# Kernel tuning notes

Hardware: AMD Instinct MI355X
Metric: run time of the kernel (lower is better)

## Reference

```python
import jax, jax.numpy as jnp
import numpy as np

WINDOW_SIZE = 11
N_CHANNELS = 3
SIGMA = 1.5
K1, K2 = 0.01, 0.03
VALUE_RANGE = 1.0


def _create_window(window_size: int, n_channels: int, sigma: float) -> np.ndarray:
    # 1D gaussian, normalized, then outer product -> 2D kernel
    coords = np.arange(window_size, dtype=np.float32) - (window_size - 1) / 2.0
    g = np.exp(-(coords ** 2) / (2.0 * sigma ** 2))
    g = g / g.sum()
    k2d = np.outer(g, g).astype(np.float32)  # (K, K), sums to 1
    # depthwise kernel, OIHW with I=1 (groups = n_channels)
    return np.broadcast_to(k2d, (n_channels, 1, window_size, window_size)).copy()


def _dwconv(x, window):
    # depthwise valid conv, NCHW / OIHW
    return jax.lax.conv_general_dilated(
        x, window, window_strides=(1, 1), padding='VALID',
        feature_group_count=window.shape[0],
        dimension_numbers=('NCHW', 'OIHW', 'NCHW'))


def setup_inputs() -> dict:
    key = jax.random.key(0)
    kx, ky = jax.random.split(key)
    N, C, H, W = 32, N_CHANNELS, 512, 512
    x = jax.random.uniform(kx, (N, C, H, W), dtype=jnp.float32)
    y = jax.random.uniform(ky, (N, C, H, W), dtype=jnp.float32)
    window = jnp.asarray(_create_window(WINDOW_SIZE, N_CHANNELS, SIGMA))
    return {"x": x, "y": y, "window": window}


def reference(x, y, window):
    c1 = (K1 * VALUE_RANGE) ** 2
    c2 = (K2 * VALUE_RANGE) ** 2

    mu_x = _dwconv(x, window)
    mu_y = _dwconv(y, window)
    mu_x_sq = mu_x ** 2
    mu_y_sq = mu_y ** 2
    mu_xy = mu_x * mu_y

    sigma_x_sq = _dwconv(x * x, window) - mu_x_sq
    sigma_y_sq = _dwconv(y * y, window) - mu_y_sq
    sigma_xy = _dwconv(x * y, window) - mu_xy

    cs = (2.0 * sigma_xy + c2) / (sigma_x_sq + sigma_y_sq + c2)
    ss = (2.0 * mu_xy + c1) / (mu_x_sq + mu_y_sq + c1) * cs

    l = ss.mean(axis=(-1, -2))  # (N, C) per-channel SSIM
    l = l.mean(axis=-1)         # (N,)  per-sample
    return l.mean()             # reduction='mean'
```

## Files before the change

kernel.cpp:

```cpp
#include <hip/hip_runtime.h>

#define KS    11
#define HH    512
#define WW    512
#define OUTD  502
#define OH    34
#define ROWS  44
#define NB    15
#define NIMG  96
#define PADW  524

__global__ __launch_bounds__(256, 2)
void ssim_main(const float* __restrict__ xg, const float* __restrict__ yg,
               const float* __restrict__ win, double* __restrict__ acc_out)
{
    __shared__ float xs[2][PADW];
    __shared__ float ys[2][PADW];
    __shared__ float wsums[4];

    const int tid  = threadIdx.x;
    const int img  = blockIdx.x % NIMG;
    const int band = blockIdx.x / NIMG;
    const int row0 = band * OH;
    const int c0   = 2 * tid;

    float g[KS];
    #pragma unroll
    for (int i = 0; i < KS; i++) {
        float s = 0.f;
        #pragma unroll
        for (int j = 0; j < KS; j++) s += win[i * KS + j];
        g[i] = s;
    }

    if (tid < (PADW - WW)) {
        xs[0][WW + tid] = 0.f; xs[1][WW + tid] = 0.f;
        ys[0][WW + tid] = 0.f; ys[1][WW + tid] = 0.f;
    }

    const float* xi = xg + (size_t)img * HH * WW;
    const float* yi = yg + (size_t)img * HH * WW;

    float acc[5][2][KS];
    #pragma unroll
    for (int q = 0; q < 5; q++)
        #pragma unroll
        for (int c = 0; c < 2; c++)
            #pragma unroll
            for (int s = 0; s < KS; s++) acc[q][c][s] = 0.f;

    float ssum = 0.f;

    const float C1 = 0.0001f;
    const float C2 = 0.0009f;

    float2 vx, vy;
    {
        int gr = row0; if (gr > HH - 1) gr = HH - 1;
        vx = *(const float2*)&xi[(size_t)gr * WW + c0];
        vy = *(const float2*)&yi[(size_t)gr * WW + c0];
        xs[0][c0] = vx.x; xs[0][c0 + 1] = vx.y;
        ys[0][c0] = vy.x; ys[0][c0 + 1] = vy.y;
        gr = row0 + 1; if (gr > HH - 1) gr = HH - 1;
        vx = *(const float2*)&xi[(size_t)gr * WW + c0];
        vy = *(const float2*)&yi[(size_t)gr * WW + c0];
    }
    __syncthreads();

    #pragma unroll 1
    for (int rb = 0; rb < ROWS / KS; rb++) {
        #pragma unroll
        for (int rr = 0; rr < KS; rr++) {
            const int r = rb * KS + rr;

            const float* xb = xs[r & 1];
            const float* yb = ys[r & 1];
            float xv[12], yv[12];
            #pragma unroll
            for (int k = 0; k < 6; k++) {
                float2 a = *(const float2*)&xb[c0 + 2 * k];
                float2 b = *(const float2*)&yb[c0 + 2 * k];
                xv[2 * k] = a.x; xv[2 * k + 1] = a.y;
                yv[2 * k] = b.x; yv[2 * k + 1] = b.y;
            }

            if (r + 1 < ROWS) {
                float* xw = xs[(r + 1) & 1];
                float* yw = ys[(r + 1) & 1];
                xw[c0] = vx.x; xw[c0 + 1] = vx.y;
                yw[c0] = vy.x; yw[c0 + 1] = vy.y;
            }
            if (r + 2 < ROWS) {
                int gr = row0 + r + 2; if (gr > HH - 1) gr = HH - 1;
                vx = *(const float2*)&xi[(size_t)gr * WW + c0];
                vy = *(const float2*)&yi[(size_t)gr * WW + c0];
            }

            float xx[12], yy[12], xy[12];
            #pragma unroll
            for (int k = 0; k < 12; k++) {
                xx[k] = xv[k] * xv[k];
                yy[k] = yv[k] * yv[k];
                xy[k] = xv[k] * yv[k];
            }

            float h[5][2];
            #pragma unroll
            for (int q = 0; q < 5; q++) { h[q][0] = 0.f; h[q][1] = 0.f; }
            #pragma unroll
            for (int j = 0; j < KS; j++) {
                const float gj = g[j];
                h[0][0] = fmaf(gj, xv[j], h[0][0]); h[0][1] = fmaf(gj, xv[j + 1], h[0][1]);
                h[1][0] = fmaf(gj, yv[j], h[1][0]); h[1][1] = fmaf(gj, yv[j + 1], h[1][1]);
                h[2][0] = fmaf(gj, xx[j], h[2][0]); h[2][1] = fmaf(gj, xx[j + 1], h[2][1]);
                h[3][0] = fmaf(gj, yy[j], h[3][0]); h[3][1] = fmaf(gj, yy[j + 1], h[3][1]);
                h[4][0] = fmaf(gj, xy[j], h[4][0]); h[4][1] = fmaf(gj, xy[j + 1], h[4][1]);
            }

            #pragma unroll
            for (int i = 0; i < KS; i++) {
                const int slot = (rr - i + KS) % KS;
                const float gi = g[i];
                #pragma unroll
                for (int q = 0; q < 5; q++) {
                    acc[q][0][slot] = fmaf(gi, h[q][0], acc[q][0][slot]);
                    acc[q][1][slot] = fmaf(gi, h[q][1], acc[q][1][slot]);
                }
            }

            const int es   = (rr + 1) % KS;
            const int jloc = r - (KS - 1);
            if (jloc >= 0 && (row0 + jloc) < OUTD) {
                #pragma unroll
                for (int c = 0; c < 2; c++) {
                    if (c0 + c < OUTD) {
                        const float mx  = acc[0][c][es], my  = acc[1][c][es];
                        const float Sxx = acc[2][c][es], Syy = acc[3][c][es], Sxy = acc[4][c][es];
                        const float mxx = mx * mx, myy = my * my, mxy = mx * my;
                        const float sxx = Sxx - mxx, syy = Syy - myy, sxy = Sxy - mxy;
                        const float num = (2.f * mxy + C1) * (2.f * sxy + C2);
                        const float den = (mxx + myy + C1) * (sxx + syy + C2);
                        float rc = __builtin_amdgcn_rcpf(den);
                        rc = rc * fmaf(-den, rc, 2.0f);
                        ssum = fmaf(num, rc, ssum);
                    }
                }
            }
            #pragma unroll
            for (int q = 0; q < 5; q++) { acc[q][0][es] = 0.f; acc[q][1][es] = 0.f; }

            __syncthreads();
        }
    }

    #pragma unroll
    for (int off = 32; off > 0; off >>= 1)
        ssum += __shfl_down(ssum, off);
    const int wave = tid >> 6;
    if ((tid & 63) == 0) wsums[wave] = ssum;
    __syncthreads();
    if (tid == 0) {
        float s = wsums[0] + wsums[1] + wsums[2] + wsums[3];
        atomicAdd(acc_out, (double)s);
    }
}

__global__ void ssim_finalize(const double* __restrict__ acc, float* __restrict__ out)
{
    out[0] = (float)(acc[0] * (1.0 / 24192384.0));
}

extern "C" void kernel_launch(void* const* d_in, const int* in_sizes, int n_in,
                              void* d_out, int out_size, void* d_ws, size_t ws_size,
                              hipStream_t stream)
{
    const float* x   = (const float*)d_in[0];
    const float* y   = (const float*)d_in[1];
    const float* win = (const float*)d_in[2];
    float* out = (float*)d_out;
    double* acc = (double*)d_ws;

    hipMemsetAsync(acc, 0, sizeof(double), stream);
    ssim_main<<<dim3(NIMG * NB), dim3(256), 0, stream>>>(x, y, win, acc);
    ssim_finalize<<<dim3(1), dim3(1), 0, stream>>>(acc, out);
}
```

Measured before the change: 278.7 us.

## Use packed float2 FMAs, one column per thread, and split images into column tiles

Each thread now handles one output column instead of two, and each image band is split into two 256-column tiles, which doubles the grid. The x and y values are interleaved into a single shared buffer of float2 pairs. The horizontal and vertical passes use packed two-wide FMAs on (x,y) pairs, which lets the compiler emit v_pk_fma_f32. Per-thread register state shrinks, so launch bounds go from 2 to 3 blocks per CU to raise occupancy. The trade-off is redundant halo loads at tile edges and fewer columns per thread to amortise the shared-memory reads.

```diff
diff --git a/kernel.cpp b/kernel.cpp
--- a/kernel.cpp
+++ b/kernel.cpp
@@ -1,4 +1,6 @@
 #include <hip/hip_runtime.h>
+
+typedef float v2f __attribute__((ext_vector_type(2)));
 
 #define KS    11
 #define HH    512
@@ -6,23 +8,26 @@
 #define OUTD  502
 #define OH    34
 #define ROWS  44
-#define NB    15
+#define NBR   15
+#define NBC   2
+#define TC    256
+#define SG    266
 #define NIMG  96
-#define PADW  524
 
-__global__ __launch_bounds__(256, 2)
+__global__ __launch_bounds__(256, 3)
 void ssim_main(const float* __restrict__ xg, const float* __restrict__ yg,
                const float* __restrict__ win, double* __restrict__ acc_out)
 {
-    __shared__ float xs[2][PADW];
-    __shared__ float ys[2][PADW];
+    __shared__ v2f buf[2][SG];
     __shared__ float wsums[4];
 
-    const int tid  = threadIdx.x;
-    const int img  = blockIdx.x % NIMG;
-    const int band = blockIdx.x / NIMG;
-    const int row0 = band * OH;
-    const int c0   = 2 * tid;
+    const int tid = threadIdx.x;
+    int bb = blockIdx.x;
+    const int img   = bb % NIMG;  bb /= NIMG;
+    const int band  = bb % NBR;   bb /= NBR;
+    const int ctile = bb;
+    const int row0  = band * OH;
+    const int cb    = ctile * TC;
 
     float g[KS];
     #pragma unroll
@@ -33,38 +38,41 @@
         g[i] = s;
     }
 
-    if (tid < (PADW - WW)) {
-        xs[0][WW + tid] = 0.f; xs[1][WW + tid] = 0.f;
-        ys[0][WW + tid] = 0.f; ys[1][WW + tid] = 0.f;
-    }
-
     const float* xi = xg + (size_t)img * HH * WW;
     const float* yi = yg + (size_t)img * HH * WW;
 
-    float acc[5][2][KS];
+    v2f   aMu[KS], aSq[KS];
+    float aXy[KS];
     #pragma unroll
-    for (int q = 0; q < 5; q++)
-        #pragma unroll
-        for (int c = 0; c < 2; c++)
-            #pragma unroll
-            for (int s = 0; s < KS; s++) acc[q][c][s] = 0.f;
+    for (int s = 0; s < KS; s++) {
+        aMu[s] = (v2f)0.f; aSq[s] = (v2f)0.f; aXy[s] = 0.f;
+    }
 
     float ssum = 0.f;
-
     const float C1 = 0.0001f;
     const float C2 = 0.0009f;
 
-    float2 vx, vy;
-    {
-        int gr = row0; if (gr > HH - 1) gr = HH - 1;
-        vx = *(const float2*)&xi[(size_t)gr * WW + c0];
-        vy = *(const float2*)&yi[(size_t)gr * WW + c0];
-        xs[0][c0] = vx.x; xs[0][c0 + 1] = vx.y;
-        ys[0][c0] = vy.x; ys[0][c0 + 1] = vy.y;
-        gr = row0 + 1; if (gr > HH - 1) gr = HH - 1;
-        vx = *(const float2*)&xi[(size_t)gr * WW + c0];
-        vy = *(const float2*)&yi[(size_t)gr * WW + c0];
-    }
+    float px0, py0, px1, py1;
+    auto load_row = [&](int r, float& x0, float& y0, float& x1, float& y1) {
+        int gr = row0 + r; if (gr > HH - 1) gr = HH - 1;
+        const size_t base = (size_t)gr * WW;
+        const int gc0 = cb + tid;
+        x0 = xi[base + gc0]; y0 = yi[base + gc0];
+        x1 = 0.f; y1 = 0.f;
+        if (tid < SG - TC) {
+            const int gc1 = cb + TC + tid;
+            if (gc1 < WW) { x1 = xi[base + gc1]; y1 = yi[base + gc1]; }
+        }
+    };
+    auto store_row = [&](int bsel, float x0, float y0, float x1, float y1) {
+        v2f v; v.x = x0; v.y = y0;
+        buf[bsel][tid] = v;
+        if (tid < SG - TC) { v2f w; w.x = x1; w.y = y1; buf[bsel][TC + tid] = w; }
+    };
+
+    load_row(0, px0, py0, px1, py1);
+    store_row(0, px0, py0, px1, py1);
+    load_row(1, px0, py0, px1, py1);
     __syncthreads();
 
     #pragma unroll 1
@@ -72,82 +80,46 @@
         #pragma unroll
         for (int rr = 0; rr < KS; rr++) {
             const int r = rb * KS + rr;
+            const v2f* bufr = buf[r & 1];
 
-            const float* xb = xs[r & 1];
-            const float* yb = ys[r & 1];
-            float xv[12], yv[12];
-            #pragma unroll
-            for (int k = 0; k < 6; k++) {
-                float2 a = *(const float2*)&xb[c0 + 2 * k];
-                float2 b = *(const float2*)&yb[c0 + 2 * k];
-                xv[2 * k] = a.x; xv[2 * k + 1] = a.y;
-                yv[2 * k] = b.x; yv[2 * k + 1] = b.y;
-            }
+            if (r + 1 < ROWS) store_row((r + 1) & 1, px0, py0, px1, py1);
+            if (r + 2 < ROWS) load_row(r + 2, px0, py0, px1, py1);
 
-            if (r + 1 < ROWS) {
-                float* xw = xs[(r + 1) & 1];
-                float* yw = ys[(r + 1) & 1];
-                xw[c0] = vx.x; xw[c0 + 1] = vx.y;
-                yw[c0] = vy.x; yw[c0 + 1] = vy.y;
-            }
-            if (r + 2 < ROWS) {
-                int gr = row0 + r + 2; if (gr > HH - 1) gr = HH - 1;
-                vx = *(const float2*)&xi[(size_t)gr * WW + c0];
-                vy = *(const float2*)&yi[(size_t)gr * WW + c0];
-            }
-
-            float xx[12], yy[12], xy[12];
-            #pragma unroll
-            for (int k = 0; k < 12; k++) {
-                xx[k] = xv[k] * xv[k];
-                yy[k] = yv[k] * yv[k];
-                xy[k] = xv[k] * yv[k];
-            }
-
-            float h[5][2];
-            #pragma unroll
-            for (int q = 0; q < 5; q++) { h[q][0] = 0.f; h[q][1] = 0.f; }
+            v2f hMu = (v2f)0.f, hSq = (v2f)0.f;
+            float hXy = 0.f;
             #pragma unroll
             for (int j = 0; j < KS; j++) {
-                const float gj = g[j];
-                h[0][0] = fmaf(gj, xv[j], h[0][0]); h[0][1] = fmaf(gj, xv[j + 1], h[0][1]);
-                h[1][0] = fmaf(gj, yv[j], h[1][0]); h[1][1] = fmaf(gj, yv[j + 1], h[1][1]);
-                h[2][0] = fmaf(gj, xx[j], h[2][0]); h[2][1] = fmaf(gj, xx[j + 1], h[2][1]);
-                h[3][0] = fmaf(gj, yy[j], h[3][0]); h[3][1] = fmaf(gj, yy[j + 1], h[3][1]);
-                h[4][0] = fmaf(gj, xy[j], h[4][0]); h[4][1] = fmaf(gj, xy[j + 1], h[4][1]);
+                const v2f v = bufr[tid + j];
+                v2f gg; gg.x = g[j]; gg.y = g[j];
+                hMu = __builtin_elementwise_fma(gg, v, hMu);
+                const v2f sq = v * v;
+                hSq = __builtin_elementwise_fma(gg, sq, hSq);
+                hXy = fmaf(g[j], v.x * v.y, hXy);
             }
 
             #pragma unroll
             for (int i = 0; i < KS; i++) {
                 const int slot = (rr - i + KS) % KS;
-                const float gi = g[i];
-                #pragma unroll
-                for (int q = 0; q < 5; q++) {
-                    acc[q][0][slot] = fmaf(gi, h[q][0], acc[q][0][slot]);
-                    acc[q][1][slot] = fmaf(gi, h[q][1], acc[q][1][slot]);
-                }
+                v2f gg; gg.x = g[i]; gg.y = g[i];
+                aMu[slot] = __builtin_elementwise_fma(gg, hMu, aMu[slot]);
+                aSq[slot] = __builtin_elementwise_fma(gg, hSq, aSq[slot]);
+                aXy[slot] = fmaf(g[i], hXy, aXy[slot]);
             }
 
             const int es   = (rr + 1) % KS;
             const int jloc = r - (KS - 1);
-            if (jloc >= 0 && (row0 + jloc) < OUTD) {
-                #pragma unroll
-                for (int c = 0; c < 2; c++) {
-                    if (c0 + c < OUTD) {
-                        const float mx  = acc[0][c][es], my  = acc[1][c][es];
-                        const float Sxx = acc[2][c][es], Syy = acc[3][c][es], Sxy = acc[4][c][es];
-                        const float mxx = mx * mx, myy = my * my, mxy = mx * my;
-                        const float sxx = Sxx - mxx, syy = Syy - myy, sxy = Sxy - mxy;
-                        const float num = (2.f * mxy + C1) * (2.f * sxy + C2);
-                        const float den = (mxx + myy + C1) * (sxx + syy + C2);
-                        float rc = __builtin_amdgcn_rcpf(den);
-                        rc = rc * fmaf(-den, rc, 2.0f);
-                        ssum = fmaf(num, rc, ssum);
-                    }
-                }
+            if (jloc >= 0 && (row0 + jloc) < OUTD && (cb + tid) < OUTD) {
+                const float mx  = aMu[es].x, my  = aMu[es].y;
+                const float Sxx = aSq[es].x, Syy = aSq[es].y, Sxy = aXy[es];
+                const float mxx = mx * mx, myy = my * my, mxy = mx * my;
+                const float sxx = Sxx - mxx, syy = Syy - myy, sxy = Sxy - mxy;
+                const float num = (2.f * mxy + C1) * (2.f * sxy + C2);
+                const float den = (mxx + myy + C1) * (sxx + syy + C2);
+                float rc = __builtin_amdgcn_rcpf(den);
+                rc = rc * fmaf(-den, rc, 2.0f);
+                ssum = fmaf(num, rc, ssum);
             }
-            #pragma unroll
-            for (int q = 0; q < 5; q++) { acc[q][0][es] = 0.f; acc[q][1][es] = 0.f; }
+            aMu[es] = (v2f)0.f; aSq[es] = (v2f)0.f; aXy[es] = 0.f;
 
             __syncthreads();
         }
@@ -181,6 +153,6 @@
     double* acc = (double*)d_ws;
 
     hipMemsetAsync(acc, 0, sizeof(double), stream);
-    ssim_main<<<dim3(NIMG * NB), dim3(256), 0, stream>>>(x, y, win, acc);
+    ssim_main<<<dim3(NIMG * NBR * NBC), dim3(256), 0, stream>>>(x, y, win, acc);
     ssim_finalize<<<dim3(1), dim3(1), 0, stream>>>(acc, out);
 }
```

Result: slower. 293.2 us (+5.2%).
